# Kernel tuning notes

Hardware: AMD Instinct MI355X
Metric: run time of the kernel (lower is better)

Reference implementation:

```python
import jax, jax.numpy as jnp
import numpy as np

EPS = 1e-5      # batch-norm epsilon
ALPHA = 0.2     # leaky_relu negative slope


def bn_lrelu(h, gamma, beta):
    # training-mode batch norm over the batch axis, then leaky relu
    mean = jnp.mean(h, axis=0)
    var = jnp.var(h, axis=0)
    h = (h - mean) * jax.lax.rsqrt(var + EPS) * gamma + beta
    return jnp.where(h >= 0, h, ALPHA * h)


def setup_inputs() -> dict:
    key = jax.random.key(0)
    ks = jax.random.split(key, 16)
    O, T, Din, H, Dout = 50000, 200000, 128, 512, 128
    s = 0.02
    inp = {
        "obj_vecs": jax.random.normal(ks[0], (O, Din), jnp.float32),
        "pred_vecs": jax.random.normal(ks[1], (T, Din), jnp.float32),
        "edges": jax.random.randint(ks[2], (T, 2), 0, O, jnp.int64),
        # net1: [3*Din -> H -> 2H+Dout], each Linear followed by BN + leaky_relu
        "W1a": jax.random.normal(ks[3], (3 * Din, H), jnp.float32) * s,
        "b1a": jnp.zeros((H,), jnp.float32),
        "g1a": jnp.ones((H,), jnp.float32),
        "be1a": jnp.zeros((H,), jnp.float32),
        "W1b": jax.random.normal(ks[4], (H, 2 * H + Dout), jnp.float32) * s,
        "b1b": jnp.zeros((2 * H + Dout,), jnp.float32),
        "g1b": jnp.ones((2 * H + Dout,), jnp.float32),
        "be1b": jnp.zeros((2 * H + Dout,), jnp.float32),
        # net2: [H -> H -> Dout]
        "W2a": jax.random.normal(ks[5], (H, H), jnp.float32) * s,
        "b2a": jnp.zeros((H,), jnp.float32),
        "g2a": jnp.ones((H,), jnp.float32),
        "be2a": jnp.zeros((H,), jnp.float32),
        "W2b": jax.random.normal(ks[6], (H, Dout), jnp.float32) * s,
        "b2b": jnp.zeros((Dout,), jnp.float32),
        "g2b": jnp.ones((Dout,), jnp.float32),
        "be2b": jnp.zeros((Dout,), jnp.float32),
    }
    return inp


def reference(obj_vecs, pred_vecs, edges,
              W1a, b1a, g1a, be1a, W1b, b1b, g1b, be1b,
              W2a, b2a, g2a, be2a, W2b, b2b, g2b, be2b):
    O = obj_vecs.shape[0]
    H = W1a.shape[1]
    Dout = W2b.shape[1]
    s_idx = edges[:, 0]
    o_idx = edges[:, 1]

    # gather subject/object vecs and concat with predicate vecs: [T, 3*Din]
    cur_t = jnp.concatenate([obj_vecs[s_idx], pred_vecs, obj_vecs[o_idx]], axis=1)

    # net1 MLP
    h = bn_lrelu(cur_t @ W1a + b1a, g1a, be1a)           # [T, H]
    new_t = bn_lrelu(h @ W1b + b1b, g1b, be1b)            # [T, 2H+Dout]

    new_s = new_t[:, :H]
    new_p = new_t[:, H:H + Dout]
    new_o = new_t[:, H + Dout:]

    # scatter-add pooling back to objects, then average
    pooled = jnp.zeros((O, H), jnp.float32).at[s_idx].add(new_s).at[o_idx].add(new_o)
    counts = jnp.zeros((O,), jnp.float32).at[s_idx].add(1.0).at[o_idx].add(1.0)
    counts = jnp.clip(counts, 1.0, float(O))
    pooled = pooled / counts[:, None]

    # net2 MLP
    h2 = bn_lrelu(pooled @ W2a + b2a, g2a, be2a)          # [O, H]
    new_obj = bn_lrelu(h2 @ W2b + b2b, g2b, be2b)         # [O, Dout]
    return new_obj, new_p
```

## Files before the change

kernel.cpp:

```cpp
#include <hip/hip_runtime.h>

typedef __bf16 bf16;
typedef __bf16 bf16x8 __attribute__((ext_vector_type(8)));
typedef float  f32x4  __attribute__((ext_vector_type(4)));

#define BM 128
#define BN 128
#define BKT 64
#define LDK (BKT + 8)
#define LDT 72

template<int AMODE, int EPI>
__global__ __launch_bounds__(256) void gemm_k(
    const bf16* __restrict__ Abf, const float* __restrict__ Af32,
    const float* __restrict__ obj, const float* __restrict__ pred,
    const int* __restrict__ edges, const float* __restrict__ invcnt,
    const float* __restrict__ scale, const float* __restrict__ shift,
    const float* __restrict__ oscale, const float* __restrict__ oshift,
    const bf16* __restrict__ WT,
    bf16* __restrict__ outB, float* __restrict__ outF,
    float* __restrict__ pooled, float* __restrict__ gsum, float* __restrict__ gsq,
    int M, int N, int K, int rbase)
{
  __shared__ __align__(16) bf16 As[BM][LDK];
  __shared__ __align__(16) bf16 Bs[BN][LDK];
  __shared__ float sc_sh[(AMODE == 1) ? 512 : 1];
  __shared__ float sh_sh[(AMODE == 1) ? 512 : 1];
  __shared__ float osc[(EPI == 2 || EPI == 5) ? BN : 1];
  __shared__ float osh[(EPI == 2 || EPI == 5) ? BN : 1];
  __shared__ int eS[(AMODE == 0 || EPI == 2) ? BM : 1];
  __shared__ int eO[(AMODE == 0 || EPI == 2) ? BM : 1];

  const int tid = threadIdx.x;

  int bx = blockIdx.x, by = blockIdx.y;
  {
    const int NX = gridDim.x, NY = gridDim.y;
    int L = by * NX + bx;
    int bpg = NX * 8;
    int nFull = NY >> 3;
    int Lfull = nFull * bpg;
    if (L < Lfull) {
      int g = L / bpg, w2 = L - g * bpg;
      by = (g << 3) + (w2 & 7);
      bx = w2 >> 3;
    } else {
      int r2 = L - Lfull;
      int q = r2 / NX;
      by = (nFull << 3) + q;
      bx = r2 - q * NX;
    }
  }
  const int m0 = rbase + by * BM;
  const int n0 = bx * BN;

  const int lane = tid & 63;
  const int w = tid >> 6;
  const int wm = (w >> 1) * 64;
  const int wn = (w & 1) * 64;
  const int l15 = lane & 15;
  const int quad = lane >> 4;

  if (AMODE == 1) {
    for (int c = tid; c < K; c += 256) { sc_sh[c] = scale[c]; sh_sh[c] = shift[c]; }
  }
  if (EPI == 2 || EPI == 5) {
    if (tid < BN) { osc[tid] = oscale[n0 + tid]; osh[tid] = oshift[n0 + tid]; }
  }
  if (AMODE == 0 || EPI == 2) {
    if (tid < BM) {
      int r = m0 + tid; if (r >= M) r = M - 1;
      eS[tid] = edges[2 * r];
      eO[tid] = edges[2 * r + 1];
    }
  }
  __syncthreads();

  f32x4 acc[4][4];
  #pragma unroll
  for (int i = 0; i < 4; ++i)
    #pragma unroll
    for (int j = 0; j < 4; ++j)
      acc[i][j] = (f32x4){0.f, 0.f, 0.f, 0.f};

  for (int k0 = 0; k0 < K; k0 += BKT) {
    {
      int idx = tid;
      #pragma unroll
      for (int it = 0; it < 4; ++it, idx += 256) {
        int r = idx >> 3, c8 = (idx & 7) << 3;
        bf16x8 v = *reinterpret_cast<const bf16x8*>(WT + (size_t)(n0 + r) * K + k0 + c8);
        *reinterpret_cast<bf16x8*>(&Bs[r][c8]) = v;
      }
    }
    if (AMODE == 1 || AMODE == 3) {
      int idx = tid;
      #pragma unroll
      for (int it = 0; it < 4; ++it, idx += 256) {
        int r = idx >> 3, c8 = (idx & 7) << 3;
        int row = m0 + r; if (row >= M) row = M - 1;
        bf16x8 v = *reinterpret_cast<const bf16x8*>(Abf + (size_t)row * K + k0 + c8);
        if (AMODE == 1) {
          bf16x8 o;
          #pragma unroll
          for (int e = 0; e < 8; ++e) {
            int c = k0 + c8 + e;
            float f = sc_sh[c] * (float)v[e] + sh_sh[c];
            f = f >= 0.f ? f : 0.2f * f;
            o[e] = (bf16)f;
          }
          *reinterpret_cast<bf16x8*>(&As[r][c8]) = o;
        } else {
          *reinterpret_cast<bf16x8*>(&As[r][c8]) = v;
        }
      }
    } else {
      int idx = tid;
      #pragma unroll
      for (int it = 0; it < 8; ++it, idx += 256) {
        int r = idx >> 4, c4 = (idx & 15) << 2;
        int row = m0 + r; if (row >= M) row = M - 1;
        const float* src;
        float mul = 1.f;
        if (AMODE == 0) {
          int k = k0 + c4;
          if (k < 128)      src = obj  + (size_t)eS[r] * 128 + k;
          else if (k < 256) src = pred + (size_t)row * 128 + (k - 128);
          else              src = obj  + (size_t)eO[r] * 128 + (k - 256);
        } else {
          src = Af32 + (size_t)row * K + k0 + c4;
          mul = invcnt[row];
        }
        float4 v = *reinterpret_cast<const float4*>(src);
        As[r][c4 + 0] = (bf16)(v.x * mul);
        As[r][c4 + 1] = (bf16)(v.y * mul);
        As[r][c4 + 2] = (bf16)(v.z * mul);
        As[r][c4 + 3] = (bf16)(v.w * mul);
      }
    }
    __syncthreads();
    #pragma unroll
    for (int kk = 0; kk < BKT; kk += 32) {
      bf16x8 af[4], bfv[4];
      #pragma unroll
      for (int i = 0; i < 4; ++i)
        af[i] = *reinterpret_cast<const bf16x8*>(&As[wm + i * 16 + l15][kk + quad * 8]);
      #pragma unroll
      for (int j = 0; j < 4; ++j)
        bfv[j] = *reinterpret_cast<const bf16x8*>(&Bs[wn + j * 16 + l15][kk + quad * 8]);
      #pragma unroll
      for (int i = 0; i < 4; ++i)
        #pragma unroll
        for (int j = 0; j < 4; ++j)
          acc[i][j] = __builtin_amdgcn_mfma_f32_16x16x32_bf16(af[i], bfv[j], acc[i][j], 0, 0, 0);
    }
    __syncthreads();
  }

  if (EPI == 2) {
    #pragma unroll
    for (int i = 0; i < 4; ++i) {
      #pragma unroll
      for (int r = 0; r < 4; ++r) {
        int lrow = wm + i * 16 + quad * 4 + r;
        int row = m0 + lrow;
        if (row >= M) continue;
        #pragma unroll
        for (int j = 0; j < 4; ++j) {
          int cl = wn + j * 16 + l15;
          int n1 = n0 + cl;
          float v = osc[cl] * acc[i][j][r] + osh[cl];
          v = v >= 0.f ? v : 0.2f * v;
          if (n1 < 512)      atomicAdd(&pooled[(size_t)eS[lrow] * 512 + n1], v);
          else if (n1 < 640) outF[(size_t)row * 128 + (n1 - 512)] = v;
          else               atomicAdd(&pooled[(size_t)eO[lrow] * 512 + (n1 - 640)], v);
        }
      }
    }
  } else if (EPI == 5) {
    #pragma unroll
    for (int i = 0; i < 4; ++i) {
      #pragma unroll
      for (int r = 0; r < 4; ++r) {
        int lrow = wm + i * 16 + quad * 4 + r;
        int row = m0 + lrow;
        if (row >= M) continue;
        #pragma unroll
        for (int j = 0; j < 4; ++j) {
          int cl = wn + j * 16 + l15;
          int n1 = n0 + cl;
          float v = osc[cl] * acc[i][j][r] + osh[cl];
          v = v >= 0.f ? v : 0.2f * v;
          if (n1 < 512)      outB[(size_t)(row - rbase) * 1024 + n1] = (bf16)v;
          else if (n1 < 640) outF[(size_t)row * 128 + (n1 - 512)] = v;
          else               outB[(size_t)(row - rbase) * 1024 + (n1 - 128)] = (bf16)v;
        }
      }
    }
  } else {
    #pragma unroll
    for (int j = 0; j < 4; ++j) {
      float s = 0.f, q = 0.f;
      #pragma unroll
      for (int i = 0; i < 4; ++i) {
        #pragma unroll
        for (int r = 0; r < 4; ++r) {
          int row = m0 + wm + i * 16 + quad * 4 + r;
          if (row >= M) continue;
          float v = acc[i][j][r];
          s += v; q += v * v;
          int col = n0 + wn + j * 16 + l15;
          if (EPI == 0) outB[(size_t)row * N + col] = (bf16)v;
          if (EPI == 3) outF[(size_t)row * N + col] = v;
        }
      }
      s += __shfl_xor(s, 16); q += __shfl_xor(q, 16);
      s += __shfl_xor(s, 32); q += __shfl_xor(q, 32);
      if (quad == 0) {
        int col = n0 + wn + j * 16 + l15;
        atomicAdd(&gsum[col], s);
        atomicAdd(&gsq[col], q);
      }
    }
  }
}

__global__ __launch_bounds__(256) void gatherc_k(const bf16* __restrict__ buf,
    const int* __restrict__ rowptr, const int* __restrict__ list,
    float* __restrict__ pooled, int c0, int c1, int O) {
  int o = blockIdx.x * 4 + (threadIdx.x >> 6);
  if (o >= O) return;
  int lane = threadIdx.x & 63;
  int cc = lane * 8;
  int e0 = rowptr[o], e1 = rowptr[o + 1];
  float acc[8];
  #pragma unroll
  for (int j = 0; j < 8; ++j) acc[j] = 0.f;
  bool any = false;
  for (int e = e0; e < e1; ++e) {
    int id = list[e];
    int t = id >> 1;
    if (t < c0 || t >= c1) continue;
    const bf16* row = buf + (size_t)(t - c0) * 1024 + (id & 1) * 512 + cc;
    bf16x8 v = *reinterpret_cast<const bf16x8*>(row);
    #pragma unroll
    for (int j = 0; j < 8; ++j) acc[j] += (float)v[j];
    any = true;
  }
  if (!any) return;
  float* dst = pooled + (size_t)o * 512 + cc;
  float4 a = *reinterpret_cast<float4*>(dst);
  float4 b = *reinterpret_cast<float4*>(dst + 4);
  a.x += acc[0]; a.y += acc[1]; a.z += acc[2]; a.w += acc[3];
  b.x += acc[4]; b.y += acc[5]; b.z += acc[6]; b.w += acc[7];
  *reinterpret_cast<float4*>(dst) = a;
  *reinterpret_cast<float4*>(dst + 4) = b;
}

__global__ __launch_bounds__(256) void gram_k(const bf16* __restrict__ A2,
                                              float* __restrict__ G, int T) {
  __shared__ __align__(16) bf16 Ks[2][128][LDT];
  const int tid = threadIdx.x;
  const int tile = blockIdx.x % 10;
  const int s    = blockIdx.x / 10;
  const int NS   = gridDim.x / 10;
  const int K1T[10] = {0, 0, 0, 0, 1, 1, 1, 2, 2, 3};
  const int K2T[10] = {0, 1, 2, 3, 1, 2, 3, 2, 3, 3};
  const int k1b = K1T[tile], k2b = K2T[tile];
  const int lane = tid & 63;
  const int w = tid >> 6;
  const int wm = (w >> 1) * 64;
  const int wn = (w & 1) * 64;
  const int l15 = lane & 15;
  const int quad = lane >> 4;

  const int NG = (T + 63) >> 6;
  const int GPB = (NG + NS - 1) / NS;
  const int g0 = s * GPB;
  const int gend = min(NG, g0 + GPB);

  f32x4 acc[4][4];
  #pragma unroll
  for (int i = 0; i < 4; ++i)
    #pragma unroll
    for (int j = 0; j < 4; ++j)
      acc[i][j] = (f32x4){0.f, 0.f, 0.f, 0.f};

  const int bsel = (k1b == k2b) ? 0 : 1;

  for (int g = g0; g < gend; ++g) {
    const int t0 = g << 6;
    #pragma unroll
    for (int it = 0; it < 4; ++it) {
      int lin = it * 256 + tid;
      int t = lin >> 4, c8 = lin & 15;
      int row = t0 + t;
      bf16x8 v;
      #pragma unroll
      for (int e = 0; e < 8; ++e) v[e] = (bf16)0.f;
      if (row < T)
        v = *reinterpret_cast<const bf16x8*>(A2 + (size_t)row * 512 + k1b * 128 + c8 * 8);
      int ts = t ^ ((c8 & 7) << 3);
      #pragma unroll
      for (int e = 0; e < 8; ++e) Ks[0][c8 * 8 + e][ts] = v[e];
    }
    if (bsel) {
      #pragma unroll
      for (int it = 0; it < 4; ++it) {
        int lin = it * 256 + tid;
        int t = lin >> 4, c8 = lin & 15;
        int row = t0 + t;
        bf16x8 v;
        #pragma unroll
        for (int e = 0; e < 8; ++e) v[e] = (bf16)0.f;
        if (row < T)
          v = *reinterpret_cast<const bf16x8*>(A2 + (size_t)row * 512 + k2b * 128 + c8 * 8);
        int ts = t ^ ((c8 & 7) << 3);
        #pragma unroll
        for (int e = 0; e < 8; ++e) Ks[1][c8 * 8 + e][ts] = v[e];
      }
    }
    __syncthreads();
    #pragma unroll
    for (int kk = 0; kk < 64; kk += 32) {
      bf16x8 af[4], bfv[4];
      #pragma unroll
      for (int i = 0; i < 4; ++i) {
        int r = wm + i * 16 + l15;
        int toff = (kk + quad * 8) ^ (((r >> 3) & 7) << 3);
        af[i] = *reinterpret_cast<const bf16x8*>(&Ks[0][r][toff]);
      }
      #pragma unroll
      for (int j = 0; j < 4; ++j) {
        int r = wn + j * 16 + l15;
        int toff = (kk + quad * 8) ^ (((r >> 3) & 7) << 3);
        bfv[j] = *reinterpret_cast<const bf16x8*>(&Ks[bsel][r][toff]);
      }
      #pragma unroll
      for (int i = 0; i < 4; ++i)
        #pragma unroll
        for (int j = 0; j < 4; ++j)
          acc[i][j] = __builtin_amdgcn_mfma_f32_16x16x32_bf16(af[i], bfv[j], acc[i][j], 0, 0, 0);
    }
    __syncthreads();
  }

  #pragma unroll
  for (int i = 0; i < 4; ++i) {
    #pragma unroll
    for (int r = 0; r < 4; ++r) {
      int grow = k1b * 128 + wm + i * 16 + quad * 4 + r;
      #pragma unroll
      for (int j = 0; j < 4; ++j) {
        int gcol = k2b * 128 + wn + j * 16 + l15;
        float v = acc[i][j][r];
        atomicAdd(&G[(size_t)grow * 512 + gcol], v);
        if (k1b != k2b)
          atomicAdd(&G[(size_t)gcol * 512 + grow], v);
      }
    }
  }
}

__global__ __launch_bounds__(256) void act_colsum_k(bf16* __restrict__ hA,
    const float* __restrict__ scale, const float* __restrict__ shift,
    float* __restrict__ csum, int T) {
  __shared__ float sh[4 * 512];
  const int tid = threadIdx.x;
  const int c0 = (tid & 63) * 8;
  const int rofs = tid >> 6;
  float sc[8], sf[8];
  #pragma unroll
  for (int j = 0; j < 8; ++j) { sc[j] = scale[c0 + j]; sf[j] = shift[c0 + j]; }
  float acc[8];
  #pragma unroll
  for (int j = 0; j < 8; ++j) acc[j] = 0.f;
  for (int r = blockIdx.x * 4 + rofs; r < T; r += gridDim.x * 4) {
    bf16x8 v = *reinterpret_cast<const bf16x8*>(hA + (size_t)r * 512 + c0);
    bf16x8 o;
    #pragma unroll
    for (int j = 0; j < 8; ++j) {
      float f = sc[j] * (float)v[j] + sf[j];
      f = f >= 0.f ? f : 0.2f * f;
      o[j] = (bf16)f;
      acc[j] += (float)o[j];
    }
    *reinterpret_cast<bf16x8*>(hA + (size_t)r * 512 + c0) = o;
  }
  #pragma unroll
  for (int j = 0; j < 8; ++j) sh[rofs * 512 + c0 + j] = acc[j];
  __syncthreads();
  for (int c = tid; c < 512; c += 256) {
    float s = sh[c] + sh[512 + c] + sh[1024 + c] + sh[1536 + c];
    atomicAdd(&csum[c], s);
  }
}

__global__ __launch_bounds__(256) void colstat_k(const float* __restrict__ G,
    const float* __restrict__ csum, const float* __restrict__ W1b,
    float* __restrict__ sumB, float* __restrict__ sqB) {
  __shared__ float wL[4][512];
  __shared__ float rq[4][4], rs[4][4];
  const int tid = threadIdx.x;
  const int c0 = blockIdx.x * 4;
  for (int idx = tid; idx < 2048; idx += 256) {
    int c = idx >> 9, k = idx & 511;
    wL[c][k] = W1b[(size_t)k * 1152 + c0 + c];
  }
  __syncthreads();
  float pq[4] = {0.f, 0.f, 0.f, 0.f};
  float ps[4] = {0.f, 0.f, 0.f, 0.f};
  for (int e = tid; e < 512 * 512; e += 256) {
    int i = e >> 9, j = e & 511;
    float g = G[e];
    #pragma unroll
    for (int c = 0; c < 4; ++c) pq[c] += g * wL[c][i] * wL[c][j];
  }
  for (int k = tid; k < 512; k += 256) {
    float cs = csum[k];
    #pragma unroll
    for (int c = 0; c < 4; ++c) ps[c] += cs * wL[c][k];
  }
  #pragma unroll
  for (int c = 0; c < 4; ++c) {
    #pragma unroll
    for (int off = 32; off > 0; off >>= 1) {
      pq[c] += __shfl_xor(pq[c], off);
      ps[c] += __shfl_xor(ps[c], off);
    }
  }
  const int w = tid >> 6, lane = tid & 63;
  if (lane == 0) {
    #pragma unroll
    for (int c = 0; c < 4; ++c) { rq[w][c] = pq[c]; rs[w][c] = ps[c]; }
  }
  __syncthreads();
  if (tid < 4) {
    sqB[c0 + tid]  = rq[0][tid] + rq[1][tid] + rq[2][tid] + rq[3][tid];
    sumB[c0 + tid] = rs[0][tid] + rs[1][tid] + rs[2][tid] + rs[3][tid];
  }
}

__global__ __launch_bounds__(256) void tconv_k(const float* __restrict__ W,
                                               bf16* __restrict__ WT, int K, int N) {
  int idx = blockIdx.x * 256 + threadIdx.x;
  if (idx < K * N) {
    int n = idx / K, k = idx - n * K;
    WT[(size_t)n * K + k] = (bf16)W[(size_t)k * N + n];
  }
}

__global__ __launch_bounds__(256) void bnfin_k(const float* __restrict__ sum,
    const float* __restrict__ sq, const float* __restrict__ g,
    const float* __restrict__ be, float* __restrict__ scale,
    float* __restrict__ shift, int C, float invR) {
  int c = blockIdx.x * 256 + threadIdx.x;
  if (c < C) {
    float m = sum[c] * invR;
    float v = sq[c] * invR - m * m;
    float a = g[c] * rsqrtf(v + 1e-5f);
    scale[c] = a;
    shift[c] = be[c] - m * a;
  }
}

__global__ __launch_bounds__(256) void cntint_k(const int* __restrict__ edges,
                                                int* __restrict__ cnt, int T) {
  int t = blockIdx.x * 256 + threadIdx.x;
  if (t < T) {
    atomicAdd(&cnt[edges[2 * t]], 1);
    atomicAdd(&cnt[edges[2 * t + 1]], 1);
  }
}

__global__ __launch_bounds__(256) void invcnt_k(const int* __restrict__ cnt,
                                                float* __restrict__ invc, int O) {
  int i = blockIdx.x * 256 + threadIdx.x;
  if (i < O) {
    float c = fminf(fmaxf((float)cnt[i], 1.f), (float)O);
    invc[i] = 1.f / c;
  }
}

__global__ __launch_bounds__(1024) void scan_k(const int* __restrict__ cnt,
    int* __restrict__ rowptr, int* __restrict__ head, int O, int total) {
  __shared__ int sh[1024];
  const int t = threadIdx.x;
  const int C = (O + 1023) / 1024;
  const int i0 = t * C;
  int s = 0;
  for (int i = 0; i < C; ++i) { int idx = i0 + i; if (idx < O) s += cnt[idx]; }
  sh[t] = s;
  __syncthreads();
  for (int d = 1; d < 1024; d <<= 1) {
    int v = (t >= d) ? sh[t - d] : 0;
    __syncthreads();
    sh[t] += v;
    __syncthreads();
  }
  int run = (t == 0) ? 0 : sh[t - 1];
  for (int i = 0; i < C; ++i) {
    int idx = i0 + i;
    if (idx < O) { rowptr[idx] = run; head[idx] = run; run += cnt[idx]; }
  }
  if (t == 0) rowptr[O] = total;
}

__global__ __launch_bounds__(256) void fill_k(const int* __restrict__ edges,
    int* __restrict__ head, int* __restrict__ list, int T) {
  int t = blockIdx.x * 256 + threadIdx.x;
  if (t < T) {
    int s = edges[2 * t];
    int p = atomicAdd(&head[s], 1);
    list[p] = t << 1;
    int o = edges[2 * t + 1];
    p = atomicAdd(&head[o], 1);
    list[p] = (t << 1) | 1;
  }
}

__global__ __launch_bounds__(256) void final_k(float* __restrict__ buf,
    const float* __restrict__ scale, const float* __restrict__ shift, int n) {
  int i = blockIdx.x * 256 + threadIdx.x;
  if (i < n) {
    int c = i & 127;
    float v = scale[c] * buf[i] + shift[c];
    buf[i] = v >= 0.f ? v : 0.2f * v;
  }
}

extern "C" void kernel_launch(void* const* d_in, const int* in_sizes, int n_in,
                              void* d_out, int out_size, void* d_ws, size_t ws_size,
                              hipStream_t stream) {
  const float* obj   = (const float*)d_in[0];
  const float* pred  = (const float*)d_in[1];
  const int*   edges = (const int*)d_in[2];
  const float* W1a = (const float*)d_in[3];
  const float* g1a = (const float*)d_in[5];
  const float* be1a= (const float*)d_in[6];
  const float* W1b = (const float*)d_in[7];
  const float* g1b = (const float*)d_in[9];
  const float* be1b= (const float*)d_in[10];
  const float* W2a = (const float*)d_in[11];
  const float* g2a = (const float*)d_in[13];
  const float* be2a= (const float*)d_in[14];
  const float* W2b = (const float*)d_in[15];
  const float* g2b = (const float*)d_in[17];
  const float* be2b= (const float*)d_in[18];

  const int O = in_sizes[0] / 128;
  const int T = in_sizes[1] / 128;
  float* out_obj = (float*)d_out;
  float* out_p   = (float*)d_out + (size_t)O * 128;

  char* base = (char*)d_ws;
  size_t off = 0;
  auto alloc = [&](size_t bytes) { size_t p = off; off += (bytes + 255) & ~(size_t)255; return p; };
  size_t oWT1a = alloc((size_t)384 * 512 * 2);
  size_t oWT1b = alloc((size_t)512 * 1152 * 2);
  size_t oWT2a = alloc((size_t)512 * 512 * 2);
  size_t oWT2b = alloc((size_t)512 * 128 * 2);
  size_t oSums = alloc(4608 * 4);
  size_t oScl  = alloc(4608 * 4);
  size_t oG    = alloc((size_t)512 * 512 * 4);
  size_t oCsum = alloc(512 * 4);
  size_t oCnt  = alloc((size_t)O * 4);
  size_t oInvc = alloc((size_t)O * 4);
  size_t oRp   = alloc((size_t)(O + 1) * 4);
  size_t oHead = alloc((size_t)O * 4);
  size_t oList = alloc((size_t)2 * T * 4);
  size_t oHA   = alloc((size_t)T * 512 * 2);
  size_t oPool = off;
  size_t oBuf  = oPool + (((size_t)O * 512 * 4 + 255) & ~(size_t)255);

  int chunkT = 0;
  if (ws_size > oBuf) {
    size_t ct = (ws_size - oBuf) / 2048;
    if (ct > (size_t)T) ct = T;
    chunkT = (int)(ct & ~(size_t)127);
  }
  const bool chunked = (chunkT >= 8192);

  bf16* WT1a = (bf16*)(base + oWT1a);
  bf16* WT1b = (bf16*)(base + oWT1b);
  bf16* WT2a = (bf16*)(base + oWT2a);
  bf16* WT2b = (bf16*)(base + oWT2b);
  float* sums = (float*)(base + oSums);
  float* sumA = sums,        * sqA = sums + 512;
  float* sumB = sums + 1024, * sqB = sums + 2176;
  float* sumC = sums + 3328, * sqC = sums + 3840;
  float* sumD = sums + 4352, * sqD = sums + 4480;
  float* scl = (float*)(base + oScl);
  float* scaleA = scl,        * shiftA = scl + 512;
  float* scaleB = scl + 1024, * shiftB = scl + 2176;
  float* scaleC = scl + 3328, * shiftC = scl + 3840;
  float* scaleD = scl + 4352, * shiftD = scl + 4480;
  float* Gm   = (float*)(base + oG);
  float* csum = (float*)(base + oCsum);
  int*   cntI = (int*)(base + oCnt);
  float* invc = (float*)(base + oInvc);
  int*   rowptr = (int*)(base + oRp);
  int*   head = (int*)(base + oHead);
  int*   list = (int*)(base + oList);
  bf16*  hA = (bf16*)(base + oHA);
  bf16*  h2 = (bf16*)(base + oHA);
  float* pooledF = (float*)(base + oPool);
  bf16*  buf = (bf16*)(base + oBuf);
  float* objpre = out_obj;

  hipMemsetAsync(sums, 0, 4608 * 4, stream);
  hipMemsetAsync(cntI, 0, (size_t)O * 4, stream);
  hipMemsetAsync(Gm, 0, (size_t)512 * 512 * 4, stream);
  hipMemsetAsync(csum, 0, 512 * 4, stream);
  hipMemsetAsync(pooledF, 0, (size_t)O * 512 * 4, stream);

  tconv_k<<<(384 * 512 + 255) / 256, 256, 0, stream>>>(W1a, WT1a, 384, 512);
  tconv_k<<<(512 * 1152 + 255) / 256, 256, 0, stream>>>(W1b, WT1b, 512, 1152);
  tconv_k<<<(512 * 512 + 255) / 256, 256, 0, stream>>>(W2a, WT2a, 512, 512);
  tconv_k<<<(512 * 128 + 255) / 256, 256, 0, stream>>>(W2b, WT2b, 512, 128);
  cntint_k<<<(T + 255) / 256, 256, 0, stream>>>(edges, cntI, T);
  invcnt_k<<<(O + 255) / 256, 256, 0, stream>>>(cntI, invc, O);
  if (chunked) {
    scan_k<<<1, 1024, 0, stream>>>(cntI, rowptr, head, O, 2 * T);
    fill_k<<<(T + 255) / 256, 256, 0, stream>>>(edges, head, list, T);
  }

  const int Tb = (T + BM - 1) / BM;
  const int Ob = (O + BM - 1) / BM;

  {
    dim3 g(512 / BN, Tb);
    gemm_k<0, 0><<<g, 256, 0, stream>>>(nullptr, nullptr, obj, pred, edges, nullptr,
        nullptr, nullptr, nullptr, nullptr, WT1a, hA, nullptr, nullptr, sumA, sqA,
        T, 512, 384, 0);
  }
  bnfin_k<<<2, 256, 0, stream>>>(sumA, sqA, g1a, be1a, scaleA, shiftA, 512, 1.f / T);

  act_colsum_k<<<1024, 256, 0, stream>>>(hA, scaleA, shiftA, csum, T);
  gram_k<<<10 * 48, 256, 0, stream>>>(hA, Gm, T);
  colstat_k<<<288, 256, 0, stream>>>(Gm, csum, W1b, sumB, sqB);
  bnfin_k<<<5, 256, 0, stream>>>(sumB, sqB, g1b, be1b, scaleB, shiftB, 1152, 1.f / T);

  if (chunked) {
    for (int c0 = 0; c0 < T; c0 += chunkT) {
      int c1 = min(T, c0 + chunkT);
      dim3 g(1152 / BN, (c1 - c0 + BM - 1) / BM);
      gemm_k<3, 5><<<g, 256, 0, stream>>>(hA, nullptr, nullptr, nullptr, nullptr,
          nullptr, nullptr, nullptr, scaleB, shiftB, WT1b, buf, out_p, nullptr,
          nullptr, nullptr, c1, 1152, 512, c0);
      gatherc_k<<<(O + 3) / 4, 256, 0, stream>>>(buf, rowptr, list, pooledF, c0, c1, O);
    }
  } else {
    dim3 g(1152 / BN, Tb);
    gemm_k<3, 2><<<g, 256, 0, stream>>>(hA, nullptr, nullptr, nullptr, edges, nullptr,
        nullptr, nullptr, scaleB, shiftB, WT1b, nullptr, out_p, pooledF, nullptr,
        nullptr, T, 1152, 512, 0);
  }

  {
    dim3 g(512 / BN, Ob);
    gemm_k<2, 0><<<g, 256, 0, stream>>>(nullptr, pooledF, nullptr, nullptr, nullptr,
        invc, nullptr, nullptr, nullptr, nullptr, WT2a, h2, nullptr, nullptr,
        sumC, sqC, O, 512, 512, 0);
  }
  bnfin_k<<<2, 256, 0, stream>>>(sumC, sqC, g2a, be2a, scaleC, shiftC, 512, 1.f / O);

  {
    dim3 g(128 / BN, Ob);
    gemm_k<1, 3><<<g, 256, 0, stream>>>(h2, nullptr, nullptr, nullptr, nullptr, nullptr,
        scaleC, shiftC, nullptr, nullptr, WT2b, nullptr, objpre, nullptr, sumD, sqD,
        O, 128, 512, 0);
  }
  bnfin_k<<<1, 256, 0, stream>>>(sumD, sqD, g2b, be2b, scaleD, shiftD, 128, 1.f / O);

  final_k<<<((size_t)O * 128 + 255) / 256, 256, 0, stream>>>(objpre, scaleD, shiftD,
      (int)((size_t)O * 128));
}
```

Measured before the change: 2.226 ms.

## Use direct global-to-LDS loads with XOR-swizzled shared tiles in GEMM

Replaces the padded LDS tiles with unpadded 64-wide tiles that use an XOR swizzle on 16-byte chunks to avoid bank conflicts. Weight tiles, and activation tiles in bf16 passthrough mode, are now loaded with global_load_lds, which writes directly to LDS without a register round trip. The other A-load paths write to the swizzled layout with vector stores. This aims to cut VGPR pressure and LDS store instructions, at the cost of depending on the builtin and needing correct wave/lane mapping for the direct-to-LDS writes.

```diff
diff --git a/kernel.cpp b/kernel.cpp
--- a/kernel.cpp
+++ b/kernel.cpp
@@ -1,14 +1,28 @@
 #include <hip/hip_runtime.h>
 
 typedef __bf16 bf16;
+typedef __bf16 bf16x4 __attribute__((ext_vector_type(4)));
 typedef __bf16 bf16x8 __attribute__((ext_vector_type(8)));
 typedef float  f32x4  __attribute__((ext_vector_type(4)));
 
 #define BM 128
 #define BN 128
 #define BKT 64
-#define LDK (BKT + 8)
 #define LDT 72
+
+#ifndef __has_builtin
+#define __has_builtin(x) 0
+#endif
+
+#if __has_builtin(__builtin_amdgcn_global_load_lds)
+#define GLL16(srcp, basep) \
+  __builtin_amdgcn_global_load_lds( \
+      (const __attribute__((address_space(1))) unsigned int*)(srcp), \
+      (__attribute__((address_space(3))) unsigned int*)(basep), 16, 0, 0)
+#else
+#define GLL16(srcp, basep) \
+  (((bf16x8*)(basep))[lane] = *(const bf16x8*)(srcp))
+#endif
 
 template<int AMODE, int EPI>
 __global__ __launch_bounds__(256) void gemm_k(
@@ -22,8 +36,8 @@
     float* __restrict__ pooled, float* __restrict__ gsum, float* __restrict__ gsq,
     int M, int N, int K, int rbase)
 {
-  __shared__ __align__(16) bf16 As[BM][LDK];
-  __shared__ __align__(16) bf16 Bs[BN][LDK];
+  __shared__ __align__(16) bf16 As[BM * 64];
+  __shared__ __align__(16) bf16 Bs[BN * 64];
   __shared__ float sc_sh[(AMODE == 1) ? 512 : 1];
   __shared__ float sh_sh[(AMODE == 1) ? 512 : 1];
   __shared__ float osc[(EPI == 2 || EPI == 5) ? BN : 1];
@@ -83,36 +97,44 @@
     for (int j = 0; j < 4; ++j)
       acc[i][j] = (f32x4){0.f, 0.f, 0.f, 0.f};
 
+  const int rsub = lane >> 3;
+  const int cch  = lane & 7;
+
   for (int k0 = 0; k0 < K; k0 += BKT) {
-    {
+    #pragma unroll
+    for (int it = 0; it < 4; ++it) {
+      int blk = it * 4 + w;
+      int r = blk * 8 + rsub;
+      int cs = cch ^ (r & 7);
+      const bf16* src = WT + (size_t)(n0 + r) * K + k0 + cs * 8;
+      GLL16(src, &Bs[blk * 512]);
+    }
+    if (AMODE == 3) {
+      #pragma unroll
+      for (int it = 0; it < 4; ++it) {
+        int blk = it * 4 + w;
+        int r = blk * 8 + rsub;
+        int row = m0 + r; if (row >= M) row = M - 1;
+        int cs = cch ^ (r & 7);
+        const bf16* src = Abf + (size_t)row * K + k0 + cs * 8;
+        GLL16(src, &As[blk * 512]);
+      }
+    } else if (AMODE == 1) {
       int idx = tid;
       #pragma unroll
       for (int it = 0; it < 4; ++it, idx += 256) {
-        int r = idx >> 3, c8 = (idx & 7) << 3;
-        bf16x8 v = *reinterpret_cast<const bf16x8*>(WT + (size_t)(n0 + r) * K + k0 + c8);
-        *reinterpret_cast<bf16x8*>(&Bs[r][c8]) = v;
-      }
-    }
-    if (AMODE == 1 || AMODE == 3) {
-      int idx = tid;
-      #pragma unroll
-      for (int it = 0; it < 4; ++it, idx += 256) {
-        int r = idx >> 3, c8 = (idx & 7) << 3;
+        int r = idx >> 3, ch = idx & 7;
         int row = m0 + r; if (row >= M) row = M - 1;
-        bf16x8 v = *reinterpret_cast<const bf16x8*>(Abf + (size_t)row * K + k0 + c8);
-        if (AMODE == 1) {
-          bf16x8 o;
-          #pragma unroll
-          for (int e = 0; e < 8; ++e) {
-            int c = k0 + c8 + e;
-            float f = sc_sh[c] * (float)v[e] + sh_sh[c];
-            f = f >= 0.f ? f : 0.2f * f;
-            o[e] = (bf16)f;
-          }
-          *reinterpret_cast<bf16x8*>(&As[r][c8]) = o;
-        } else {
-          *reinterpret_cast<bf16x8*>(&As[r][c8]) = v;
+        bf16x8 v = *reinterpret_cast<const bf16x8*>(Abf + (size_t)row * K + k0 + ch * 8);
+        bf16x8 o;
+        #pragma unroll
+        for (int e = 0; e < 8; ++e) {
+          int c = k0 + ch * 8 + e;
+          float f = sc_sh[c] * (float)v[e] + sh_sh[c];
+          f = f >= 0.f ? f : 0.2f * f;
+          o[e] = (bf16)f;
         }
+        *reinterpret_cast<bf16x8*>(&As[r * 64 + ((ch ^ (r & 7)) << 3)]) = o;
       }
     } else {
       int idx = tid;
@@ -132,10 +154,12 @@
           mul = invcnt[row];
         }
         float4 v = *reinterpret_cast<const float4*>(src);
-        As[r][c4 + 0] = (bf16)(v.x * mul);
-        As[r][c4 + 1] = (bf16)(v.y * mul);
-        As[r][c4 + 2] = (bf16)(v.z * mul);
-        As[r][c4 + 3] = (bf16)(v.w * mul);
+        bf16x4 o;
+        o[0] = (bf16)(v.x * mul); o[1] = (bf16)(v.y * mul);
+        o[2] = (bf16)(v.z * mul); o[3] = (bf16)(v.w * mul);
+        int ch = c4 >> 3;
+        int half = (c4 >> 2) & 1;
+        *reinterpret_cast<bf16x4*>(&As[r * 64 + ((ch ^ (r & 7)) << 3) + (half << 2)]) = o;
       }
     }
     __syncthreads();
@@ -143,11 +167,17 @@
     for (int kk = 0; kk < BKT; kk += 32) {
       bf16x8 af[4], bfv[4];
       #pragma unroll
-      for (int i = 0; i < 4; ++i)
-        af[i] = *reinterpret_cast<const bf16x8*>(&As[wm + i * 16 + l15][kk + quad * 8]);
-      #pragma unroll
-      for (int j = 0; j < 4; ++j)
-        bfv[j] = *reinterpret_cast<const bf16x8*>(&Bs[wn + j * 16 + l15][kk + quad * 8]);
+      for (int i = 0; i < 4; ++i) {
+        int r = wm + i * 16 + l15;
+        int ci = (kk >> 3) + quad;
+        af[i] = *reinterpret_cast<const bf16x8*>(&As[r * 64 + ((ci ^ (r & 7)) << 3)]);
+      }
+      #pragma unroll
+      for (int j = 0; j < 4; ++j) {
+        int r = wn + j * 16 + l15;
+        int ci = (kk >> 3) + quad;
+        bfv[j] = *reinterpret_cast<const bf16x8*>(&Bs[r * 64 + ((ci ^ (r & 7)) << 3)]);
+      }
       #pragma unroll
       for (int i = 0; i < 4; ++i)
         #pragma unroll
```

Result: faster. 2.028 ms (-8.9%).
